# Performance work log

Hardware: AMD Instinct MI355X
Metric: run time of the kernel (lower is better)

The kernel has to match this reference:

```python
import jax, jax.numpy as jnp
import numpy as np

N_STATE = 512
M_IN = 64
P_OUT = 64
BATCH = 32
SEQ = 2048


def setup_inputs() -> dict:
    key = jax.random.key(0)
    k1, k2, k3, k4, k5 = jax.random.split(key, 5)
    u = jax.random.normal(k1, (BATCH, SEQ, M_IN), dtype=jnp.float32)
    # CompanionParam init: a ~ randn * 0.01 (keeps companion matrix stable, near shift matrix)
    a = jax.random.normal(k2, (N_STATE,), dtype=jnp.float32) * 0.01
    B = jax.random.normal(k3, (N_STATE, M_IN), dtype=jnp.float32) * 0.05
    C = jax.random.normal(k4, (P_OUT, N_STATE), dtype=jnp.float32) * 0.05
    D = jax.random.normal(k5, (P_OUT, M_IN), dtype=jnp.float32) * 0.05
    return {"u": u, "a": a, "B": B, "C": C, "D": D}


def companion_matrix(a):
    # A[i+1, i] = 1 on subdiagonal; last column = -flip(a)  (matches CompanionParam.matrix)
    n = a.shape[0]
    idx = jnp.arange(n - 1)
    A = jnp.zeros((n, n), dtype=a.dtype)
    A = A.at[idx + 1, idx].set(1.0)
    A = A.at[:, n - 1].set(-a[::-1])
    return A


def reference(u, a, B, C, D):
    # LTI SSM recurrence: x_t = A x_{t-1} + B u_t ; y_t = C x_t + D u_t
    A = companion_matrix(a)  # (n, n)
    batch, T, m = u.shape
    n = a.shape[0]
    u_t = jnp.transpose(u, (1, 0, 2))  # (T, batch, m)
    Bu = jnp.einsum('tbm,nm->tbn', u_t, B)  # precompute input drive (T, batch, n)

    def step(x, bu):
        x_new = x @ A.T + bu  # (batch, n)
        return x_new, x_new

    x0 = jnp.zeros((batch, n), dtype=u.dtype)
    _, xs = jax.lax.scan(step, x0, Bu)  # xs: (T, batch, n)
    ys = jnp.einsum('tbn,pn->tbp', xs, C) + jnp.einsum('tbm,pm->tbp', u_t, D)
    return jnp.transpose(ys, (1, 0, 2))  # (batch, T, p)
```

## Files before the change

### kernel.cpp

```cpp
#include <hip/hip_runtime.h>

#define SEQ  2048
#define NB   32
#define NS   512
#define MI   64
#define PO   64
#define TB   64
#define NTB  32
#define CH   64
#define NCH  8
#define LDU  72
#define LDD  66
#define SG_LDA 72

typedef __attribute__((ext_vector_type(8))) __bf16 bf16x8;
typedef __attribute__((ext_vector_type(4))) float  floatx4;

__device__ inline unsigned short f2bf(float f) {
    unsigned u = __builtin_bit_cast(unsigned, f);
    u += 0x7fff + ((u >> 16) & 1);
    return (unsigned short)(u >> 16);
}

__global__ void __launch_bounds__(256) prep_all_kernel(
    const float* __restrict__ u, const float* __restrict__ B,
    const float* __restrict__ C, const float* __restrict__ D,
    const float* __restrict__ a,
    unsigned short* __restrict__ ubf, unsigned short* __restrict__ BflatT,
    unsigned short* __restrict__ Bws, unsigned short* __restrict__ Cws,
    unsigned short* __restrict__ Dws, unsigned short* __restrict__ qT) {
    __shared__ float a_ext[1024];
    const int bx = blockIdx.x, tid = threadIdx.x;
    if (bx < 2048) {
        const size_t base = ((size_t)bx * 256 + tid) * 8;
        float4 f0 = *(const float4*)(u + base);
        float4 f1 = *(const float4*)(u + base + 4);
        unsigned short tmp[8];
        tmp[0] = f2bf(f0.x); tmp[1] = f2bf(f0.y); tmp[2] = f2bf(f0.z); tmp[3] = f2bf(f0.w);
        tmp[4] = f2bf(f1.x); tmp[5] = f2bf(f1.y); tmp[6] = f2bf(f1.z); tmp[7] = f2bf(f1.w);
        *(uint4*)(ubf + base) = *(uint4*)&tmp[0];
    } else if (bx < 2560) {
        const int i = bx - 2048;
        for (int r = 0; r < 2; ++r) {
            const int id = tid + r * 256;
            const int j = id >> 3, q8 = (id & 7) * 8;
            unsigned short tmp[8];
            if (i >= j) {
                const float4 f0 = *(const float4*)(B + (size_t)(i - j) * MI + q8);
                const float4 f1 = *(const float4*)(B + (size_t)(i - j) * MI + q8 + 4);
                tmp[0] = f2bf(f0.x); tmp[1] = f2bf(f0.y); tmp[2] = f2bf(f0.z); tmp[3] = f2bf(f0.w);
                tmp[4] = f2bf(f1.x); tmp[5] = f2bf(f1.y); tmp[6] = f2bf(f1.z); tmp[7] = f2bf(f1.w);
            } else {
#pragma unroll
                for (int z = 0; z < 8; ++z) tmp[z] = 0;
            }
            *(uint4*)(BflatT + (size_t)i * 4096 + j * 64 + q8) = *(uint4*)&tmp[0];
        }
    } else if (bx < 2624) {
        const int p = bx - 2560;
        for (int x = tid; x < 1024; x += 256) a_ext[x] = (x < NS) ? a[x] : 0.f;
        __syncthreads();
        const int j0 = tid, j1 = tid + 256;
        float acc0 = 0.f, acc1 = 0.f;
        const float4* crow = (const float4*)(C + (size_t)p * NS);
        for (int i4 = 0; i4 < NS / 4; ++i4) {
            const float4 cv = crow[i4];
            const int base = 511 - i4 * 4;
            acc0 += cv.x * a_ext[base + j0]     + cv.y * a_ext[base - 1 + j0] +
                    cv.z * a_ext[base - 2 + j0] + cv.w * a_ext[base - 3 + j0];
            acc1 += cv.x * a_ext[base + j1]     + cv.y * a_ext[base - 1 + j1] +
                    cv.z * a_ext[base - 2 + j1] + cv.w * a_ext[base - 3 + j1];
        }
        qT[(size_t)p * NS + j0] = f2bf(acc0);
        qT[(size_t)p * NS + j1] = f2bf(acc1);
    } else {
        const int idx = (bx - 2624) * 256 + tid;
        const int nB = NS * MI, nC = PO * NS, nD = PO * MI;
        if (idx < nB) Bws[idx] = f2bf(B[idx]);
        else if (idx < nB + nC) Cws[idx - nB] = f2bf(C[idx - nB]);
        else if (idx < nB + nC + nD) Dws[idx - nB - nC] = f2bf(D[idx - nB - nC]);
    }
}

__global__ void __launch_bounds__(256) sgemm_kernel(const unsigned short* __restrict__ ubf,
                                                    const unsigned short* __restrict__ BflatT,
                                                    float* __restrict__ Sbuf) {
    __shared__ unsigned short A_l[4 * 64 * SG_LDA];
    __shared__ unsigned short U_l[4 * 32 * SG_LDA];
    const int ib = blockIdx.x, b = blockIdx.y;
    const int tid = threadIdx.x, lane = tid & 63, w = tid >> 6;
    const int row16 = lane & 15, quad = lane >> 4;
    const int i0 = ib * 64;
    floatx4 acc[2];
#pragma unroll
    for (int ns = 0; ns < 2; ++ns) acc[ns] = (floatx4){0.f, 0.f, 0.f, 0.f};

    for (int jg = 0; jg < 16; ++jg) {
#pragma unroll
        for (int r = 0; r < 8; ++r) {
            const int id = tid + r * 256;
            const int row = id >> 5;
            const int jj = (id >> 3) & 3, q8 = (id & 7) * 8;
            const int j = jg * 4 + jj;
            *(uint4*)&A_l[(jj * 64 + row) * SG_LDA + q8] =
                *(const uint4*)(BflatT + (size_t)(i0 + row) * 4096 + j * 64 + q8);
        }
#pragma unroll
        for (int r = 0; r < 4; ++r) {
            const int id = tid + r * 256;
            const int n = id >> 5;
            const int jj = (id >> 3) & 3, q8 = (id & 7) * 8;
            const int j = jg * 4 + jj;
            *(uint4*)&U_l[(jj * 32 + n) * SG_LDA + q8] =
                *(const uint4*)(ubf + ((size_t)b * SEQ + n * 64 + 63 - j) * MI + q8);
        }
        __syncthreads();
#pragma unroll
        for (int jj = 0; jj < 4; ++jj) {
#pragma unroll
            for (int mk = 0; mk < 2; ++mk) {
                const bf16x8 av = *(const bf16x8*)
                    &A_l[(jj * 64 + w * 16 + row16) * SG_LDA + mk * 32 + quad * 8];
#pragma unroll
                for (int ns = 0; ns < 2; ++ns) {
                    const bf16x8 bv = *(const bf16x8*)
                        &U_l[(jj * 32 + ns * 16 + row16) * SG_LDA + mk * 32 + quad * 8];
                    acc[ns] = __builtin_amdgcn_mfma_f32_16x16x32_bf16(av, bv, acc[ns], 0, 0, 0);
                }
            }
        }
        __syncthreads();
    }
#pragma unroll
    for (int ns = 0; ns < 2; ++ns) {
        const int n = ns * 16 + row16;
        float* dst = Sbuf + ((size_t)b * NTB + n) * NS + i0 + w * 16 + quad * 4;
        *(floatx4*)dst = acc[ns];
    }
}

__global__ void __launch_bounds__(1024) scan_himp_kernel(const float* __restrict__ Sbuf,
                                                         float* __restrict__ Rbuf,
                                                         const float* __restrict__ a,
                                                         float* __restrict__ hbuf) {
    __shared__ __align__(16) char smem[24576];
    const int tid = threadIdx.x;
    if (blockIdx.x < NB) {
        const int b = blockIdx.x;
        const float4* S4 = (const float4*)(Sbuf + (size_t)b * NTB * NS);
        float4* R4 = (float4*)(Rbuf + (size_t)b * NTB * NS);
        for (int o = tid; o < NTB * NS / 4; o += 1024) {
            const int k = o >> 7;
            const int i4 = o & 127;
            float4 acc = make_float4(0.f, 0.f, 0.f, 0.f);
#pragma unroll
            for (int m = 0; m < 8; ++m) {
                if (m <= k - 1 && i4 >= 16 * m) {
                    const float4 s = S4[(k - 1 - m) * 128 + i4 - 16 * m];
                    acc.x += s.x; acc.y += s.y; acc.z += s.z; acc.w += s.w;
                }
            }
            R4[o] = acc;
        }
    } else {
        float* a_l     = (float*)smem;
        float* h_ext   = (float*)(smem + 2560);
        float* part    = (float*)(smem + 12800);
        float* rhs_ext = (float*)(smem + 20992);
        const int kk = tid & 63, grp = tid >> 6;

        for (int x = tid; x < 640; x += 1024) a_l[x] = (x < NS) ? a[x] : 0.f;
        for (int x = tid; x < 640; x += 1024) h_ext[x] = 0.f;
        if (tid < 256) rhs_ext[tid] = 0.f;
        __syncthreads();

        float aw[34];
#pragma unroll
        for (int i = 0; i < 34; ++i) aw[i] = a_l[2 * kk + grp * 32 + i];

        if (tid < 64) {
            if (tid == 0) h_ext[512] = 1.f;
            float acc = (tid >= 1) ? a_l[tid - 1] : 0.f;
            for (int s = 1; s < 64; ++s) {
                const float hs = -__shfl(acc, s);
                if (tid == s) h_ext[512 + s] = hs;
                const float av = a_l[(tid > s) ? (tid - 1 - s) : 0];
                acc += (tid > s) ? av * hs : 0.f;
            }
        }
        __syncthreads();

        int t0 = 64;
        while (t0 < SEQ) {
            float acc0 = 0.f, acc1 = 0.f;
#pragma unroll
            for (int m = 0; m < 8; ++m) {
                const float4 hv = *(const float4*)&h_ext[512 + t0 - grp * 32 - 4 - 4 * m];
                acc0 += aw[4 * m + 0] * hv.w + aw[4 * m + 1] * hv.z +
                        aw[4 * m + 2] * hv.y + aw[4 * m + 3] * hv.x;
                acc1 += aw[4 * m + 1] * hv.w + aw[4 * m + 2] * hv.z +
                        aw[4 * m + 3] * hv.y + aw[4 * m + 4] * hv.x;
            }
            *(float2*)&part[grp * 128 + 2 * kk] = make_float2(acc0, acc1);
            __syncthreads();
            if (tid < 128) {
                float r = 0.f;
#pragma unroll
                for (int g = 0; g < 16; ++g) r += part[g * 128 + tid];
                rhs_ext[128 + tid] = -r;
            }
            __syncthreads();
            {
                const int g = tid >> 7, out = tid & 127;
                const int k0 = g * 16;
                float s = 0.f;
#pragma unroll
                for (int k4 = 0; k4 < 4; ++k4) {
                    const float4 h4 = *(const float4*)&h_ext[512 + k0 + 4 * k4];
                    const int base = 128 + out - k0 - 4 * k4;
                    s += h4.x * rhs_ext[base]     + h4.y * rhs_ext[base - 1] +
                         h4.z * rhs_ext[base - 2] + h4.w * rhs_ext[base - 3];
                }
                part[g * 128 + out] = s;
            }
            __syncthreads();
            if (tid < 128) {
                float r = 0.f;
#pragma unroll
                for (int g = 0; g < 8; ++g) r += part[g * 128 + tid];
                h_ext[512 + t0 + tid] = r;
            }
            __syncthreads();
            t0 += (t0 == 64) ? 64 : 128;
        }
        for (int i = tid; i < SEQ; i += 1024) hbuf[i] = h_ext[512 + i];
    }
}

__global__ void __launch_bounds__(256) ytile_kernel(
    const unsigned short* __restrict__ ubf, const unsigned short* __restrict__ Bws,
    const unsigned short* __restrict__ Cws, const unsigned short* __restrict__ Dws,
    const float* __restrict__ Rbuf, float* __restrict__ fbuf, float* __restrict__ y) {
    __shared__ unsigned short u_b[TB * LDU];
    __shared__ float buDiag[TB * LDD];
    __shared__ unsigned short Gb[TB * LDU];
    __shared__ float colBuf[2][TB];

    const int blk = blockIdx.x, b = blockIdx.y;
    const int t0 = blk * TB;
    const int tid = threadIdx.x;
    const int lane = tid & 63, w = tid >> 6;
    const int row16 = lane & 15, quad = lane >> 4;
    const size_t rbase = ((size_t)b * NTB + blk) * NS;

#pragma unroll
    for (int r = 0; r < 2; ++r) {
        const int id = tid + r * 256;
        const int t = id >> 3, q8 = (id & 7) * 8;
        *(uint4*)&u_b[t * LDU + q8] =
            *(const uint4*)(ubf + ((size_t)b * SEQ + t0 + t) * MI + q8);
    }
    if (tid < TB) colBuf[0][tid] = 0.f;

    floatx4 accY[4];
#pragma unroll
    for (int nt = 0; nt < 4; ++nt) accY[nt] = (floatx4){0.f, 0.f, 0.f, 0.f};
    __syncthreads();

    bf16x8 ufr0[4], ufr1[4];
#pragma unroll
    for (int nt = 0; nt < 4; ++nt) {
        const int t = nt * 16 + row16;
        ufr0[nt] = *(const bf16x8*)&u_b[t * LDU + quad * 8];
        ufr1[nt] = *(const bf16x8*)&u_b[t * LDU + 32 + quad * 8];
    }

    int cur = 0;
    for (int ch = 0; ch < NCH; ++ch) {
        const bf16x8 bf0 = *(const bf16x8*)(Bws + (size_t)(ch * CH + w * 16 + row16) * MI + quad * 8);
        const bf16x8 bf1 = *(const bf16x8*)(Bws + (size_t)(ch * CH + w * 16 + row16) * MI + 32 + quad * 8);
        const bf16x8 cf0 = *(const bf16x8*)(Cws + (size_t)(w * 16 + row16) * NS + ch * CH + quad * 8);
        const bf16x8 cf1 = *(const bf16x8*)(Cws + (size_t)(w * 16 + row16) * NS + ch * CH + 32 + quad * 8);

#pragma unroll
        for (int nt = 0; nt < 4; ++nt) {
            floatx4 dacc = {0.f, 0.f, 0.f, 0.f};
            dacc = __builtin_amdgcn_mfma_f32_16x16x32_bf16(bf0, ufr0[nt], dacc, 0, 0, 0);
            dacc = __builtin_amdgcn_mfma_f32_16x16x32_bf16(bf1, ufr1[nt], dacc, 0, 0, 0);
            const int t = nt * 16 + row16;
            const int ibase = w * 16 + quad * 4;
#pragma unroll
            for (int r = 0; r < 4; ++r) {
                const int dd = (ibase + r - t) & 63;
                buDiag[dd * LDD + t] = dacc[r];
            }
        }
        __syncthreads();

        const int nxt = cur ^ 1;
        if (tid < 64) {
            const int d = tid;
            const int gi = ch * CH + d;
            float run = (gi >= 1) ? Rbuf[rbase + gi - 1] : 0.f;
            const float carryB = (ch > 0) ? colBuf[cur][d] : 0.f;
            const int tsplit = 63 - d;
            float exitVal = 0.f;
#pragma unroll 4
            for (int k = 0; k < 32; ++k) {
                const float2 tv = *(const float2*)&buDiag[d * LDD + 2 * k];
                {
                    const int t = 2 * k;
                    run += tv.x;
                    Gb[t * LDU + ((d + t) & 63)] = f2bf(run);
                    const bool sp = (t == tsplit);
                    exitVal = sp ? run : exitVal;
                    run = sp ? carryB : run;
                }
                {
                    const int t = 2 * k + 1;
                    run += tv.y;
                    Gb[t * LDU + ((d + t) & 63)] = f2bf(run);
                    const bool sp = (t == tsplit);
                    exitVal = sp ? run : exitVal;
                    run = sp ? carryB : run;
                }
            }
            if (ch == NCH - 1) fbuf[(size_t)b * SEQ + t0 + tsplit] = exitVal;
            else colBuf[nxt][d] = exitVal;
        }
        __syncthreads();

#pragma unroll
        for (int nt = 0; nt < 4; ++nt) {
            const int t = nt * 16 + row16;
            bf16x8 g0 = *(const bf16x8*)&Gb[t * LDU + quad * 8];
            bf16x8 g1 = *(const bf16x8*)&Gb[t * LDU + 32 + quad * 8];
            accY[nt] = __builtin_amdgcn_mfma_f32_16x16x32_bf16(cf0, g0, accY[nt], 0, 0, 0);
            accY[nt] = __builtin_amdgcn_mfma_f32_16x16x32_bf16(cf1, g1, accY[nt], 0, 0, 0);
        }
        __syncthreads();
        cur = nxt;
    }

    const bf16x8 df0 = *(const bf16x8*)(Dws + (size_t)(w * 16 + row16) * MI + quad * 8);
    const bf16x8 df1 = *(const bf16x8*)(Dws + (size_t)(w * 16 + row16) * MI + 32 + quad * 8);
#pragma unroll
    for (int nt = 0; nt < 4; ++nt) {
        const int t = nt * 16 + row16;
        accY[nt] = __builtin_amdgcn_mfma_f32_16x16x32_bf16(df0, ufr0[nt], accY[nt], 0, 0, 0);
        accY[nt] = __builtin_amdgcn_mfma_f32_16x16x32_bf16(df1, ufr1[nt], accY[nt], 0, 0, 0);
        const int p0 = w * 16 + quad * 4;
        *(floatx4*)(y + ((size_t)b * SEQ + t0 + t) * PO + p0) = accY[nt];
    }
}

__global__ void __launch_bounds__(256) sconv_kernel(const float* __restrict__ fbuf,
                                                    const float* __restrict__ hbuf,
                                                    float* __restrict__ sbuf) {
    __shared__ float f_l[SEQ];
    __shared__ float h_lc[SEQ + 8];
    __shared__ float part[4][TB];
    const int blk = blockIdx.x, b = blockIdx.y, tid = threadIdx.x;
    const int t0 = blk * TB;
    const int len = t0 + TB;
    {
        const float4* fs = (const float4*)(fbuf + (size_t)b * SEQ);
        const float4* hs = (const float4*)hbuf;
        for (int i = tid; i < len / 4; i += 256) {
            ((float4*)f_l)[i] = fs[i];
            ((float4*)h_lc)[i] = hs[i];
        }
    }
    __syncthreads();
    const int dt = tid & 63, grp = tid >> 6;
    const int t = t0 + dt;
    float acc = 0.f;
    for (int j4 = grp * 4; j4 <= t; j4 += 16) {
        const float4 hv = *(const float4*)&h_lc[j4];
        if (j4 + 0 <= t) acc += hv.x * f_l[t - j4 - 0];
        if (j4 + 1 <= t) acc += hv.y * f_l[t - j4 - 1];
        if (j4 + 2 <= t) acc += hv.z * f_l[t - j4 - 2];
        if (j4 + 3 <= t) acc += hv.w * f_l[t - j4 - 3];
    }
    part[grp][dt] = acc;
    __syncthreads();
    if (tid < TB) {
        sbuf[(size_t)b * SEQ + t0 + tid] =
            part[0][tid] + part[1][tid] + part[2][tid] + part[3][tid];
    }
}

__global__ void __launch_bounds__(256) corr_kernel(
    const float* __restrict__ sbuf, const unsigned short* __restrict__ qT,
    float* __restrict__ y) {
    __shared__ float s_l[NS + TB];
    __shared__ unsigned short Sw[2][TB * LDU];
    const int blk = blockIdx.x, b = blockIdx.y, tid = threadIdx.x;
    const int t0 = blk * TB;
    const int lane = tid & 63, w = tid >> 6;
    const int row16 = lane & 15, quad = lane >> 4;
    for (int idx = tid; idx < NS + TB; idx += 256) {
        const int t = t0 - NS + idx;
        s_l[idx] = (t >= 0) ? sbuf[(size_t)b * SEQ + t] : 0.f;
    }
    floatx4 acc[4];
#pragma unroll
    for (int nt = 0; nt < 4; ++nt) acc[nt] = (floatx4){0.f, 0.f, 0.f, 0.f};
    __syncthreads();

    for (int ch = 0; ch < NCH; ++ch) {
        const int buf = ch & 1;
        const bf16x8 qf0 = *(const bf16x8*)(qT + (size_t)(w * 16 + row16) * NS + ch * CH + quad * 8);
        const bf16x8 qf1 = *(const bf16x8*)(qT + (size_t)(w * 16 + row16) * NS + ch * CH + 32 + quad * 8);
        {
            const int r = tid >> 2, c0 = (tid & 3) * 16;
            unsigned short tmp[16];
            const int base = 511 + r - ch * CH - c0;
#pragma unroll
            for (int jj = 0; jj < 16; ++jj) tmp[jj] = f2bf(s_l[base - jj]);
            *(uint4*)&Sw[buf][r * LDU + c0]     = *(uint4*)&tmp[0];
            *(uint4*)&Sw[buf][r * LDU + c0 + 8] = *(uint4*)&tmp[8];
        }
        __syncthreads();
#pragma unroll
        for (int nt = 0; nt < 4; ++nt) {
            const int t = nt * 16 + row16;
            bf16x8 s0 = *(const bf16x8*)&Sw[buf][t * LDU + quad * 8];
            bf16x8 s1 = *(const bf16x8*)&Sw[buf][t * LDU + 32 + quad * 8];
            acc[nt] = __builtin_amdgcn_mfma_f32_16x16x32_bf16(qf0, s0, acc[nt], 0, 0, 0);
            acc[nt] = __builtin_amdgcn_mfma_f32_16x16x32_bf16(qf1, s1, acc[nt], 0, 0, 0);
        }
    }
#pragma unroll
    for (int nt = 0; nt < 4; ++nt) {
        const int t = nt * 16 + row16;
        const int p0 = w * 16 + quad * 4;
        float* yp = y + ((size_t)b * SEQ + t0 + t) * PO + p0;
        floatx4 old = *(const floatx4*)yp;
        *(floatx4*)yp = old - acc[nt];
    }
}

extern "C" void kernel_launch(void* const* d_in, const int* in_sizes, int n_in,
                              void* d_out, int out_size, void* d_ws,
                              size_t ws_size, hipStream_t stream) {
    const float* u  = (const float*)d_in[0];
    const float* a  = (const float*)d_in[1];
    const float* B  = (const float*)d_in[2];
    const float* Cm = (const float*)d_in[3];
    const float* Dm = (const float*)d_in[4];
    float* y = (float*)d_out;

    char* ws = (char*)d_ws;
    unsigned short* Bws = (unsigned short*)ws;                  ws += NS * MI * 2;
    unsigned short* Cws = (unsigned short*)ws;                  ws += PO * NS * 2;
    unsigned short* Dws = (unsigned short*)ws;                  ws += PO * MI * 2;
    unsigned short* qTw = (unsigned short*)ws;                  ws += PO * NS * 2;
    unsigned short* ubf = (unsigned short*)ws;                  ws += (size_t)NB * SEQ * MI * 2;
    unsigned short* Bft = (unsigned short*)ws;                  ws += (size_t)NS * 4096 * 2;
    float* Sbuf = (float*)ws;                                   ws += (size_t)NB * NTB * NS * 4;
    float* Rbuf = (float*)ws;                                   ws += (size_t)NB * NTB * NS * 4;
    float* fbuf = (float*)ws;                                   ws += (size_t)NB * SEQ * 4;
    float* sbuf = (float*)ws;                                   ws += (size_t)NB * SEQ * 4;
    float* hbuf = (float*)ws;

    prep_all_kernel<<<dim3(2896), dim3(256), 0, stream>>>(
        u, B, Cm, Dm, a, ubf, Bft, Bws, Cws, Dws, qTw);
    sgemm_kernel<<<dim3(8, 32), dim3(256), 0, stream>>>(ubf, Bft, Sbuf);
    scan_himp_kernel<<<dim3(NB + 1), dim3(1024), 0, stream>>>(Sbuf, Rbuf, a, hbuf);
    ytile_kernel<<<dim3(NTB, NB), dim3(256), 0, stream>>>(
        ubf, Bws, Cws, Dws, Rbuf, fbuf, y);
    sconv_kernel<<<dim3(NTB, NB), dim3(256), 0, stream>>>(fbuf, hbuf, sbuf);
    corr_kernel<<<dim3(NTB, NB), dim3(256), 0, stream>>>(sbuf, qTw, y);
}
```

Baseline: 222.7 us.

## Parallelize diagonal prefix scan across all four waves in ytile kernel

Replaces the serial 64-step running sum done by a single wave with a two-level scan. All 256 threads each compute a 16-element local prefix, then combine group offsets through shared memory, and a split-point exit value is broadcast. It also prefetches the next chunk's Rbuf seed, drops one barrier per chunk, pads buDiag to 68 for float4 reads, and sets a launch-bounds occupancy hint. The exchange is extra barriers and shared-memory traffic per chunk, plus register pressure from the 16-value prefix array.

```diff
diff --git a/kernel.cpp b/kernel.cpp
--- a/kernel.cpp
+++ b/kernel.cpp
@@ -10,7 +10,7 @@
 #define CH   64
 #define NCH  8
 #define LDU  72
-#define LDD  66
+#define LDD  68
 #define SG_LDA 72
 
 typedef __attribute__((ext_vector_type(8))) __bf16 bf16x8;
@@ -237,21 +237,28 @@
     }
 }
 
-__global__ void __launch_bounds__(256) ytile_kernel(
+__global__ void __launch_bounds__(256, 4) ytile_kernel(
     const unsigned short* __restrict__ ubf, const unsigned short* __restrict__ Bws,
     const unsigned short* __restrict__ Cws, const unsigned short* __restrict__ Dws,
     const float* __restrict__ Rbuf, float* __restrict__ fbuf, float* __restrict__ y) {
     __shared__ unsigned short u_b[TB * LDU];
     __shared__ float buDiag[TB * LDD];
     __shared__ unsigned short Gb[TB * LDU];
-    __shared__ float colBuf[2][TB];
+    __shared__ float sgrp[4][TB];
+    __shared__ float psplitL[TB];
+    __shared__ float exitBuf[2][TB];
 
     const int blk = blockIdx.x, b = blockIdx.y;
     const int t0 = blk * TB;
     const int tid = threadIdx.x;
     const int lane = tid & 63, w = tid >> 6;
     const int row16 = lane & 15, quad = lane >> 4;
+    const int dsc = lane;
+    const int g = w;
     const size_t rbase = ((size_t)b * NTB + blk) * NS;
+    const int tsplit = 63 - dsc, gsplit = tsplit >> 4, jsplit = tsplit & 15;
+
+    float sA = (dsc >= 1) ? Rbuf[rbase + dsc - 1] : 0.f;
 
 #pragma unroll
     for (int r = 0; r < 2; ++r) {
@@ -260,7 +267,6 @@
         *(uint4*)&u_b[t * LDU + q8] =
             *(const uint4*)(ubf + ((size_t)b * SEQ + t0 + t) * MI + q8);
     }
-    if (tid < TB) colBuf[0][tid] = 0.f;
 
     floatx4 accY[4];
 #pragma unroll
@@ -277,6 +283,9 @@
 
     int cur = 0;
     for (int ch = 0; ch < NCH; ++ch) {
+        float sA_next = 0.f;
+        if (ch + 1 < NCH) sA_next = Rbuf[rbase + (ch + 1) * 64 + dsc - 1];
+
         const bf16x8 bf0 = *(const bf16x8*)(Bws + (size_t)(ch * CH + w * 16 + row16) * MI + quad * 8);
         const bf16x8 bf1 = *(const bf16x8*)(Bws + (size_t)(ch * CH + w * 16 + row16) * MI + 32 + quad * 8);
         const bf16x8 cf0 = *(const bf16x8*)(Cws + (size_t)(w * 16 + row16) * NS + ch * CH + quad * 8);
@@ -297,36 +306,49 @@
         }
         __syncthreads();
 
-        const int nxt = cur ^ 1;
-        if (tid < 64) {
-            const int d = tid;
-            const int gi = ch * CH + d;
-            float run = (gi >= 1) ? Rbuf[rbase + gi - 1] : 0.f;
-            const float carryB = (ch > 0) ? colBuf[cur][d] : 0.f;
-            const int tsplit = 63 - d;
-            float exitVal = 0.f;
-#pragma unroll 4
-            for (int k = 0; k < 32; ++k) {
-                const float2 tv = *(const float2*)&buDiag[d * LDD + 2 * k];
-                {
-                    const int t = 2 * k;
-                    run += tv.x;
-                    Gb[t * LDU + ((d + t) & 63)] = f2bf(run);
-                    const bool sp = (t == tsplit);
-                    exitVal = sp ? run : exitVal;
-                    run = sp ? carryB : run;
-                }
-                {
-                    const int t = 2 * k + 1;
-                    run += tv.y;
-                    Gb[t * LDU + ((d + t) & 63)] = f2bf(run);
-                    const bool sp = (t == tsplit);
-                    exitVal = sp ? run : exitVal;
-                    run = sp ? carryB : run;
-                }
-            }
-            if (ch == NCH - 1) fbuf[(size_t)b * SEQ + t0 + tsplit] = exitVal;
-            else colBuf[nxt][d] = exitVal;
+        float pv[16];
+        {
+            const float* row = &buDiag[dsc * LDD + g * 16];
+            const float4 v0 = *(const float4*)(row + 0);
+            const float4 v1 = *(const float4*)(row + 4);
+            const float4 v2 = *(const float4*)(row + 8);
+            const float4 v3 = *(const float4*)(row + 12);
+            pv[0]  = v0.x;          pv[1]  = pv[0]  + v0.y;
+            pv[2]  = pv[1]  + v0.z; pv[3]  = pv[2]  + v0.w;
+            pv[4]  = pv[3]  + v1.x; pv[5]  = pv[4]  + v1.y;
+            pv[6]  = pv[5]  + v1.z; pv[7]  = pv[6]  + v1.w;
+            pv[8]  = pv[7]  + v2.x; pv[9]  = pv[8]  + v2.y;
+            pv[10] = pv[9]  + v2.z; pv[11] = pv[10] + v2.w;
+            pv[12] = pv[11] + v3.x; pv[13] = pv[12] + v3.y;
+            pv[14] = pv[13] + v3.z; pv[15] = pv[14] + v3.w;
+        }
+        sgrp[g][dsc] = pv[15];
+        __syncthreads();
+
+        const float s0 = sgrp[0][dsc], s1 = sgrp[1][dsc], s2 = sgrp[2][dsc];
+        const float off = (g > 0 ? s0 : 0.f) + (g > 1 ? s1 : 0.f) + (g > 2 ? s2 : 0.f);
+        float plocal = pv[0];
+#pragma unroll
+        for (int j = 1; j < 16; ++j) plocal = (j == jsplit) ? pv[j] : plocal;
+        if (g == gsplit) {
+            const float Ps = off + plocal;
+            psplitL[dsc] = Ps;
+            const float ev = sA + Ps;
+            if (ch == NCH - 1) fbuf[(size_t)b * SEQ + t0 + tsplit] = ev;
+            else exitBuf[cur ^ 1][dsc] = ev;
+        }
+        __syncthreads();
+
+        {
+            const float Ps = psplitL[dsc];
+            const float cB = (ch > 0) ? exitBuf[cur][dsc] : 0.f;
+#pragma unroll
+            for (int j = 0; j < 16; ++j) {
+                const int t = g * 16 + j;
+                const float incl = off + pv[j];
+                const float out = (t <= tsplit) ? (sA + incl) : (cB + (incl - Ps));
+                Gb[t * LDU + ((dsc + t) & 63)] = f2bf(out);
+            }
         }
         __syncthreads();
 
@@ -338,8 +360,8 @@
             accY[nt] = __builtin_amdgcn_mfma_f32_16x16x32_bf16(cf0, g0, accY[nt], 0, 0, 0);
             accY[nt] = __builtin_amdgcn_mfma_f32_16x16x32_bf16(cf1, g1, accY[nt], 0, 0, 0);
         }
-        __syncthreads();
-        cur = nxt;
+        sA = sA_next;
+        cur ^= 1;
     }
 
     const bf16x8 df0 = *(const bf16x8*)(Dws + (size_t)(w * 16 + row16) * MI + quad * 8);
```

New measurement: 220.4 us. No clear change (-1.0%).
